# Kernel optimization log

Measured on AMD Instinct MI355X. Metric: run time of the kernel, lower is better.

## Reference

```python
import jax, jax.numpy as jnp
import numpy as np
from jax import lax

N_VOX = 100000   # occupied voxels
GRID = 160       # dense grid extent per axis
K = 5            # kernel size -> 125 offsets
K3 = K * K * K
IMG_C, PTS_C, OUT_C = 64, 32, 16
EPS = 1e-5


def _build_coords_and_kernel_map():
    """Random unique voxel coords + kernel map: nbr[n,k] = row index of voxel at
    coords[n]+offset[k], or N_VOX (sentinel -> zero feature) if unoccupied."""
    rng = np.random.default_rng(0)
    flat = rng.choice(GRID ** 3, size=N_VOX, replace=False)
    coords = np.stack(np.unravel_index(flat, (GRID, GRID, GRID)), axis=1).astype(np.int64)
    B = GRID + 4  # shift coords by +2 so offsets in [-2,2] never wrap
    enc = ((coords[:, 0] + 2) * B + (coords[:, 1] + 2)) * B + (coords[:, 2] + 2)
    order = np.argsort(enc)
    enc_s = enc[order]
    offs = np.stack(np.meshgrid(np.arange(-2, 3), np.arange(-2, 3), np.arange(-2, 3), indexing='ij'), axis=-1).reshape(-1, 3)
    nbr = np.full((N_VOX, K3), N_VOX, dtype=np.int32)
    for k, (dx, dy, dz) in enumerate(offs):
        qe = enc + ((dx * B + dy) * B + dz)
        pos = np.clip(np.searchsorted(enc_s, qe), 0, N_VOX - 1)
        hit = enc_s[pos] == qe
        nbr[:, k] = np.where(hit, order[pos].astype(np.int32), np.int32(N_VOX))
    return nbr


def setup_inputs() -> dict:
    nbr_idx = jnp.asarray(_build_coords_and_kernel_map())
    key = jax.random.key(0)
    ks = jax.random.split(key, 20)
    def w(k, shape, fan):
        return jax.random.normal(k, shape, jnp.float32) * (1.0 / np.sqrt(fan))
    def bn(k0, k1, k2, k3):
        g = jax.random.uniform(k0, (OUT_C,), jnp.float32) + 0.5
        b = jax.random.normal(k1, (OUT_C,), jnp.float32) * 0.1
        m = jax.random.normal(k2, (OUT_C,), jnp.float32) * 0.1
        v = jax.random.uniform(k3, (OUT_C,), jnp.float32) + 0.5
        return g, b, m, v
    bn_img = bn(ks[2], ks[3], ks[4], ks[5])
    bn_pts = bn(ks[7], ks[8], ks[9], ks[10])
    bn_vis = bn(ks[12], ks[13], ks[14], ks[15])
    return {
        'img_voxel_feats': jax.random.normal(ks[0], (N_VOX, IMG_C), jnp.float32),
        'pts_voxel_feats': jax.random.normal(ks[1], (N_VOX, PTS_C), jnp.float32),
        'nbr_idx': nbr_idx,
        'W_img': w(ks[16], (K3, IMG_C, OUT_C), K3 * IMG_C),
        'bn_img_g': bn_img[0], 'bn_img_b': bn_img[1], 'bn_img_m': bn_img[2], 'bn_img_v': bn_img[3],
        'W_pts': w(ks[17], (K3, PTS_C, OUT_C), K3 * PTS_C),
        'bn_pts_g': bn_pts[0], 'bn_pts_b': bn_pts[1], 'bn_pts_m': bn_pts[2], 'bn_pts_v': bn_pts[3],
        'W_vis1': w(ks[18], (K3, 2 * OUT_C, OUT_C), K3 * 2 * OUT_C),
        'bn_vis_g': bn_vis[0], 'bn_vis_b': bn_vis[1], 'bn_vis_m': bn_vis[2], 'bn_vis_v': bn_vis[3],
        'W_vis2': w(ks[19], (OUT_C, 1), OUT_C),
    }


def _sparse_conv(feats, W, nbr_idx):
    # gather-GEMM-scatter sparse conv; sentinel row N -> zero feature
    feats_pad = jnp.concatenate([feats, jnp.zeros((1, feats.shape[1]), feats.dtype)], axis=0)
    init = jnp.zeros((feats.shape[0], W.shape[2]), feats.dtype)
    def step(acc, wk_ik):
        W_k, idx_k = wk_ik  # [Cin,Cout], [N]
        return acc + feats_pad[idx_k] @ W_k, None
    out, _ = lax.scan(step, init, (W, nbr_idx.T))
    return out


def _bn_relu(x, g, b, m, v):
    return jax.nn.relu((x - m) * (g * lax.rsqrt(v + EPS)) + b)


def reference(img_voxel_feats, pts_voxel_feats, nbr_idx,
              W_img, bn_img_g, bn_img_b, bn_img_m, bn_img_v,
              W_pts, bn_pts_g, bn_pts_b, bn_pts_m, bn_pts_v,
              W_vis1, bn_vis_g, bn_vis_b, bn_vis_m, bn_vis_v,
              W_vis2):
    img = _bn_relu(_sparse_conv(img_voxel_feats, W_img, nbr_idx), bn_img_g, bn_img_b, bn_img_m, bn_img_v)
    pts = _bn_relu(_sparse_conv(pts_voxel_feats, W_pts, nbr_idx), bn_pts_g, bn_pts_b, bn_pts_m, bn_pts_v)
    cat = jnp.concatenate([img, pts], axis=1)  # [N, 2*OUT_C]
    h = _bn_relu(_sparse_conv(cat, W_vis1, nbr_idx), bn_vis_g, bn_vis_b, bn_vis_m, bn_vis_v)
    vis_w = jax.nn.sigmoid(h @ W_vis2)  # [N,1]
    return vis_w * img + (1.0 - vis_w) * pts
```

## Files before the change

kernel.cpp:

```cpp
#include <hip/hip_runtime.h>

#define N_VOX 100000
#define K3 125
#define CENTER_K 62
#define CAP 4096
#define EPSF 1e-5f

#define CNT 0
#define PRS 2048
#define ACC (2048 + 2 * 125 * CAP)
#define ACV (ACC + N_VOX * 32)
#define CAT (ACV + N_VOX * 16)

__global__ __launch_bounds__(256) void build_pairs(const int* __restrict__ nbr,
                                                   float* __restrict__ ws)
{
    int* cnt = (int*)(ws + CNT);
    int2* pairs = (int2*)(ws + PRS);
    const int TOT4 = (N_VOX * K3) / 4;
    const int4* n4 = (const int4*)nbr;
    for (int i4 = blockIdx.x * 256 + threadIdx.x; i4 < TOT4; i4 += gridDim.x * 256) {
        int4 v = n4[i4];
        int base = i4 * 4;
        int idxs[4] = {v.x, v.y, v.z, v.w};
        #pragma unroll
        for (int j = 0; j < 4; ++j) {
            int idx = idxs[j];
            int i = base + j;
            int n = i / K3;
            int k = i - n * K3;
            if (idx < N_VOX && k != CENTER_K) {
                int pos = atomicAdd(&cnt[k * 16], 1);
                if (pos < CAP) pairs[(size_t)k * CAP + pos] = make_int2(n, idx);
            }
        }
    }
}

__device__ __forceinline__ void loadFA(float4 (&F)[12], int2 pr,
    const float4* __restrict__ fi4, const float4* __restrict__ fp4, int h)
{
    const float4* fi = fi4 + (size_t)pr.y * 16 + h * 8;
    const float4* fp = fp4 + (size_t)pr.y * 8 + h * 4;
    #pragma unroll
    for (int j = 0; j < 8; ++j) F[j] = fi[j];
    #pragma unroll
    for (int j = 0; j < 4; ++j) F[8 + j] = fp[j];
}

__device__ __forceinline__ void computeFA(const float4 (&F)[12],
    const float (&Wi)[32], const float (&Wp)[16], float& aI, float& aP)
{
    float a0 = 0.f, a1 = 0.f, b0 = 0.f, b1 = 0.f;
    #pragma unroll
    for (int j = 0; j < 4; ++j) {
        float4 f = F[j];
        a0 += f.x*Wi[4*j] + f.y*Wi[4*j+1] + f.z*Wi[4*j+2] + f.w*Wi[4*j+3];
        float4 g = F[4 + j];
        a1 += g.x*Wi[16+4*j] + g.y*Wi[16+4*j+1] + g.z*Wi[16+4*j+2] + g.w*Wi[16+4*j+3];
    }
    #pragma unroll
    for (int j = 0; j < 2; ++j) {
        float4 f = F[8 + j];
        b0 += f.x*Wp[4*j] + f.y*Wp[4*j+1] + f.z*Wp[4*j+2] + f.w*Wp[4*j+3];
        float4 g = F[10 + j];
        b1 += g.x*Wp[8+4*j] + g.y*Wp[8+4*j+1] + g.z*Wp[8+4*j+2] + g.w*Wp[8+4*j+3];
    }
    aI = a0 + a1; aP = b0 + b1;
}

__global__ __launch_bounds__(256) void scatterA(
    const float* __restrict__ fimg, const float* __restrict__ fpts,
    const float* __restrict__ Wimg, const float* __restrict__ Wpts,
    float* __restrict__ ws)
{
    const int k = blockIdx.x;
    const int lane = threadIdx.x & 63;
    const int wv = threadIdx.x >> 6;
    const int s = lane >> 5;
    const int h = (lane >> 4) & 1;
    const int o = lane & 15;

    float Wi[32];
    #pragma unroll
    for (int j = 0; j < 32; ++j) Wi[j] = Wimg[k * 1024 + (h * 32 + j) * 16 + o];
    float Wp[16];
    #pragma unroll
    for (int j = 0; j < 16; ++j) Wp[j] = Wpts[k * 512 + (h * 16 + j) * 16 + o];

    int cnt = ((const int*)(ws + CNT))[k * 16];
    if (cnt > CAP) cnt = CAP;
    const int2* __restrict__ pairs = (const int2*)(ws + PRS) + (size_t)k * CAP;
    float* __restrict__ acc = ws + ACC;
    const float4* __restrict__ fi4 = (const float4*)fimg;
    const float4* __restrict__ fp4 = (const float4*)fpts;

    const int S = gridDim.y * 8;
    int p = (blockIdx.y * 4 + wv) * 2 + s;

    int2 prA = make_int2(0, 0), prB = make_int2(0, 0);
    if (p < cnt) prA = pairs[p];
    if (p + S < cnt) prB = pairs[p + S];
    float4 FA[12], FB[12];
    loadFA(FA, prA, fi4, fp4, h);

    while (p < cnt) {
        {
            int2 prC = make_int2(0, 0);
            if (p + 2 * S < cnt) prC = pairs[p + 2 * S];
            loadFA(FB, prB, fi4, fp4, h);
            float aI, aP;
            computeFA(FA, Wi, Wp, aI, aP);
            aI += __shfl_xor(aI, 16); aP += __shfl_xor(aP, 16);
            atomicAdd(&acc[(size_t)prA.x * 32 + h * 16 + o], h ? aP : aI);
            p += S; prA = prB; prB = prC;
        }
        if (p >= cnt) break;
        {
            int2 prC = make_int2(0, 0);
            if (p + 2 * S < cnt) prC = pairs[p + 2 * S];
            loadFA(FA, prB, fi4, fp4, h);
            float aI, aP;
            computeFA(FB, Wi, Wp, aI, aP);
            aI += __shfl_xor(aI, 16); aP += __shfl_xor(aP, 16);
            atomicAdd(&acc[(size_t)prA.x * 32 + h * 16 + o], h ? aP : aI);
            p += S; prA = prB; prB = prC;
        }
    }
}

__device__ __forceinline__ void loadFV(float4 (&F)[8], int2 pr,
    const float4* __restrict__ c4)
{
    const float4* cr = c4 + (size_t)pr.y * 8;
    #pragma unroll
    for (int j = 0; j < 8; ++j) F[j] = cr[j];
}

__device__ __forceinline__ void computeFV(const float4 (&F)[8],
    const float (&Wv)[32], float& aV)
{
    float a0 = 0.f, a1 = 0.f;
    #pragma unroll
    for (int j = 0; j < 4; ++j) {
        float4 f = F[j];
        a0 += f.x*Wv[4*j] + f.y*Wv[4*j+1] + f.z*Wv[4*j+2] + f.w*Wv[4*j+3];
        float4 g = F[4 + j];
        a1 += g.x*Wv[16+4*j] + g.y*Wv[16+4*j+1] + g.z*Wv[16+4*j+2] + g.w*Wv[16+4*j+3];
    }
    aV = a0 + a1;
}

__global__ __launch_bounds__(256) void scatterV(
    const float* __restrict__ Wvis, float* __restrict__ ws)
{
    const int k = blockIdx.x;
    const int lane = threadIdx.x & 63;
    const int wv = threadIdx.x >> 6;
    const int s = lane >> 4;
    const int o = lane & 15;

    float Wv[32];
    #pragma unroll
    for (int j = 0; j < 32; ++j) Wv[j] = Wvis[k * 512 + j * 16 + o];

    int cnt = ((const int*)(ws + CNT))[k * 16];
    if (cnt > CAP) cnt = CAP;
    const int2* __restrict__ pairs = (const int2*)(ws + PRS) + (size_t)k * CAP;
    const float4* __restrict__ c4 = (const float4*)(ws + CAT);
    float* __restrict__ accV = ws + ACV;

    const int S = gridDim.y * 16;
    int p = (blockIdx.y * 4 + wv) * 4 + s;

    int2 prA = make_int2(0, 0), prB = make_int2(0, 0);
    if (p < cnt) prA = pairs[p];
    if (p + S < cnt) prB = pairs[p + S];
    float4 FA[8], FB[8];
    loadFV(FA, prA, c4);

    while (p < cnt) {
        {
            int2 prC = make_int2(0, 0);
            if (p + 2 * S < cnt) prC = pairs[p + 2 * S];
            loadFV(FB, prB, c4);
            float aV; computeFV(FA, Wv, aV);
            atomicAdd(&accV[(size_t)prA.x * 16 + o], aV);
            p += S; prA = prB; prB = prC;
        }
        if (p >= cnt) break;
        {
            int2 prC = make_int2(0, 0);
            if (p + 2 * S < cnt) prC = pairs[p + 2 * S];
            loadFV(FA, prB, c4);
            float aV; computeFV(FB, Wv, aV);
            atomicAdd(&accV[(size_t)prA.x * 16 + o], aV);
            p += S; prA = prB; prB = prC;
        }
    }
}

__global__ __launch_bounds__(256) void finalizeA(
    const float* __restrict__ fimg, const float* __restrict__ fpts,
    const float* __restrict__ Wimg, const float* __restrict__ Wpts,
    float* __restrict__ ws,
    const float* __restrict__ gi, const float* __restrict__ bi,
    const float* __restrict__ mi, const float* __restrict__ vi,
    const float* __restrict__ gp, const float* __restrict__ bp,
    const float* __restrict__ mp, const float* __restrict__ vp)
{
    int o = threadIdx.x & 15;
    int slot = threadIdx.x >> 4;
    float Wi_r[64];
    #pragma unroll
    for (int c = 0; c < 64; ++c) Wi_r[c] = Wimg[CENTER_K * 1024 + c * 16 + o];
    float Wp_r[32];
    #pragma unroll
    for (int c = 0; c < 32; ++c) Wp_r[c] = Wpts[CENTER_K * 512 + c * 16 + o];
    float sI = gi[o] * rsqrtf(vi[o] + EPSF), bI = bi[o], mI = mi[o];
    float sP = gp[o] * rsqrtf(vp[o] + EPSF), bP = bp[o], mP = mp[o];

    const float4* __restrict__ fi4 = (const float4*)fimg;
    const float4* __restrict__ fp4 = (const float4*)fpts;
    const float* __restrict__ acc = ws + ACC;
    float* __restrict__ cat = ws + CAT;

    for (int n = blockIdx.x * 16 + slot; n < N_VOX; n += gridDim.x * 16) {
        const float4* fr = fi4 + (size_t)n * 16;
        const float4* gr = fp4 + (size_t)n * 8;
        float aI0 = 0.f, aI1 = 0.f, aP0 = 0.f, aP1 = 0.f;
        #pragma unroll
        for (int t = 0; t < 8; ++t) {
            float4 f = fr[t];
            aI0 += f.x*Wi_r[4*t] + f.y*Wi_r[4*t+1] + f.z*Wi_r[4*t+2] + f.w*Wi_r[4*t+3];
            float4 g = fr[8 + t];
            aI1 += g.x*Wi_r[32+4*t] + g.y*Wi_r[32+4*t+1] + g.z*Wi_r[32+4*t+2] + g.w*Wi_r[32+4*t+3];
        }
        #pragma unroll
        for (int t = 0; t < 4; ++t) {
            float4 f = gr[t];
            aP0 += f.x*Wp_r[4*t] + f.y*Wp_r[4*t+1] + f.z*Wp_r[4*t+2] + f.w*Wp_r[4*t+3];
            float4 g = gr[4 + t];
            aP1 += g.x*Wp_r[16+4*t] + g.y*Wp_r[16+4*t+1] + g.z*Wp_r[16+4*t+2] + g.w*Wp_r[16+4*t+3];
        }
        float tI = acc[(size_t)n * 32 + o] + aI0 + aI1;
        float tP = acc[(size_t)n * 32 + 16 + o] + aP0 + aP1;
        cat[(size_t)n * 32 + o]      = fmaxf((tI - mI) * sI + bI, 0.f);
        cat[(size_t)n * 32 + 16 + o] = fmaxf((tP - mP) * sP + bP, 0.f);
    }
}

__global__ __launch_bounds__(256) void finalizeB(
    const float* __restrict__ Wvis, float* __restrict__ ws,
    const float* __restrict__ gv, const float* __restrict__ bv,
    const float* __restrict__ mv, const float* __restrict__ vv,
    const float* __restrict__ w2, float* __restrict__ out)
{
    int o = threadIdx.x & 15;
    int slot = threadIdx.x >> 4;
    float Wv_r[32];
    #pragma unroll
    for (int c = 0; c < 32; ++c) Wv_r[c] = Wvis[CENTER_K * 512 + c * 16 + o];
    float sV = gv[o] * rsqrtf(vv[o] + EPSF), bV = bv[o], mV = mv[o], w2_ = w2[o];

    const float4* __restrict__ c4 = (const float4*)(ws + CAT);
    const float* __restrict__ cat = ws + CAT;
    const float* __restrict__ accV = ws + ACV;

    for (int n = blockIdx.x * 16 + slot; n < N_VOX; n += gridDim.x * 16) {
        const float4* cr = c4 + (size_t)n * 8;
        float a0 = 0.f, a1 = 0.f;
        #pragma unroll
        for (int t = 0; t < 4; ++t) {
            float4 f = cr[t];
            a0 += f.x*Wv_r[4*t] + f.y*Wv_r[4*t+1] + f.z*Wv_r[4*t+2] + f.w*Wv_r[4*t+3];
            float4 g = cr[4 + t];
            a1 += g.x*Wv_r[16+4*t] + g.y*Wv_r[16+4*t+1] + g.z*Wv_r[16+4*t+2] + g.w*Wv_r[16+4*t+3];
        }
        float tV = accV[(size_t)n * 16 + o] + a0 + a1;
        float h = fmaxf((tV - mV) * sV + bV, 0.f);
        float ph = h * w2_;
        ph += __shfl_xor(ph, 1); ph += __shfl_xor(ph, 2);
        ph += __shfl_xor(ph, 4); ph += __shfl_xor(ph, 8);
        float vis = 1.f / (1.f + expf(-ph));
        float xi = cat[(size_t)n * 32 + o];
        float xp = cat[(size_t)n * 32 + 16 + o];
        out[(size_t)n * 16 + o] = vis * xi + (1.f - vis) * xp;
    }
}

extern "C" void kernel_launch(void* const* d_in, const int* in_sizes, int n_in,
                              void* d_out, int out_size, void* d_ws, size_t ws_size,
                              hipStream_t stream) {
    const float* fimg = (const float*)d_in[0];
    const float* fpts = (const float*)d_in[1];
    const int*   nbr  = (const int*)d_in[2];
    const float* Wimg = (const float*)d_in[3];
    const float* gi = (const float*)d_in[4];
    const float* bi = (const float*)d_in[5];
    const float* mi = (const float*)d_in[6];
    const float* vi = (const float*)d_in[7];
    const float* Wpts = (const float*)d_in[8];
    const float* gp = (const float*)d_in[9];
    const float* bp = (const float*)d_in[10];
    const float* mp = (const float*)d_in[11];
    const float* vp = (const float*)d_in[12];
    const float* Wvis = (const float*)d_in[13];
    const float* gv = (const float*)d_in[14];
    const float* bv = (const float*)d_in[15];
    const float* mv = (const float*)d_in[16];
    const float* vv = (const float*)d_in[17];
    const float* w2 = (const float*)d_in[18];
    float* out = (float*)d_out;
    float* ws = (float*)d_ws;

    hipMemsetAsync(ws + CNT, 0, 2048 * sizeof(float), stream);
    hipMemsetAsync(ws + ACC, 0, (size_t)N_VOX * 48 * sizeof(float), stream);

    hipLaunchKernelGGL(build_pairs, dim3(4096), dim3(256), 0, stream, nbr, ws);
    hipLaunchKernelGGL(scatterA, dim3(125, 8), dim3(256), 0, stream,
                       fimg, fpts, Wimg, Wpts, ws);
    hipLaunchKernelGGL(finalizeA, dim3(1024), dim3(256), 0, stream,
                       fimg, fpts, Wimg, Wpts, ws, gi, bi, mi, vi, gp, bp, mp, vp);
    hipLaunchKernelGGL(scatterV, dim3(125, 8), dim3(256), 0, stream, Wvis, ws);
    hipLaunchKernelGGL(finalizeB, dim3(1024), dim3(256), 0, stream,
                       Wvis, ws, gv, bv, mv, vv, w2, out);
}
```

Measured before the change: 205.6 us.

## Split channel reduction across more lanes and quadruple scatter grid for occupancy

In scatterA each pair is now handled by a full wave, with four lane groups each reducing a quarter of the input channels and combining them through two shuffles, instead of half-waves with two groups. scatterV likewise splits its channels across two lane groups. The double-buffered software prefetch of feature rows is dropped, which shrinks register arrays, and launch bounds ask for 8 blocks per SM. The grid y-dimension grows from 8 to 32, so more waves are in flight to hide gather latency. The cost is more shuffles, idle lanes during the atomics, and no explicit prefetch of the next feature row.

```diff
diff --git a/kernel.cpp b/kernel.cpp
--- a/kernel.cpp
+++ b/kernel.cpp
@@ -37,39 +37,7 @@
     }
 }
 
-__device__ __forceinline__ void loadFA(float4 (&F)[12], int2 pr,
-    const float4* __restrict__ fi4, const float4* __restrict__ fp4, int h)
-{
-    const float4* fi = fi4 + (size_t)pr.y * 16 + h * 8;
-    const float4* fp = fp4 + (size_t)pr.y * 8 + h * 4;
-    #pragma unroll
-    for (int j = 0; j < 8; ++j) F[j] = fi[j];
-    #pragma unroll
-    for (int j = 0; j < 4; ++j) F[8 + j] = fp[j];
-}
-
-__device__ __forceinline__ void computeFA(const float4 (&F)[12],
-    const float (&Wi)[32], const float (&Wp)[16], float& aI, float& aP)
-{
-    float a0 = 0.f, a1 = 0.f, b0 = 0.f, b1 = 0.f;
-    #pragma unroll
-    for (int j = 0; j < 4; ++j) {
-        float4 f = F[j];
-        a0 += f.x*Wi[4*j] + f.y*Wi[4*j+1] + f.z*Wi[4*j+2] + f.w*Wi[4*j+3];
-        float4 g = F[4 + j];
-        a1 += g.x*Wi[16+4*j] + g.y*Wi[16+4*j+1] + g.z*Wi[16+4*j+2] + g.w*Wi[16+4*j+3];
-    }
-    #pragma unroll
-    for (int j = 0; j < 2; ++j) {
-        float4 f = F[8 + j];
-        b0 += f.x*Wp[4*j] + f.y*Wp[4*j+1] + f.z*Wp[4*j+2] + f.w*Wp[4*j+3];
-        float4 g = F[10 + j];
-        b1 += g.x*Wp[8+4*j] + g.y*Wp[8+4*j+1] + g.z*Wp[8+4*j+2] + g.w*Wp[8+4*j+3];
-    }
-    aI = a0 + a1; aP = b0 + b1;
-}
-
-__global__ __launch_bounds__(256) void scatterA(
+__global__ __launch_bounds__(256, 8) void scatterA(
     const float* __restrict__ fimg, const float* __restrict__ fpts,
     const float* __restrict__ Wimg, const float* __restrict__ Wpts,
     float* __restrict__ ws)
@@ -77,16 +45,15 @@
     const int k = blockIdx.x;
     const int lane = threadIdx.x & 63;
     const int wv = threadIdx.x >> 6;
-    const int s = lane >> 5;
-    const int h = (lane >> 4) & 1;
+    const int q = lane >> 4;
     const int o = lane & 15;
 
-    float Wi[32];
-    #pragma unroll
-    for (int j = 0; j < 32; ++j) Wi[j] = Wimg[k * 1024 + (h * 32 + j) * 16 + o];
-    float Wp[16];
-    #pragma unroll
-    for (int j = 0; j < 16; ++j) Wp[j] = Wpts[k * 512 + (h * 16 + j) * 16 + o];
+    float Wi[16];
+    #pragma unroll
+    for (int j = 0; j < 16; ++j) Wi[j] = Wimg[k * 1024 + (q * 16 + j) * 16 + o];
+    float Wp[8];
+    #pragma unroll
+    for (int j = 0; j < 8; ++j) Wp[j] = Wpts[k * 512 + (q * 8 + j) * 16 + o];
 
     int cnt = ((const int*)(ws + CNT))[k * 16];
     if (cnt > CAP) cnt = CAP;
@@ -95,74 +62,49 @@
     const float4* __restrict__ fi4 = (const float4*)fimg;
     const float4* __restrict__ fp4 = (const float4*)fpts;
 
-    const int S = gridDim.y * 8;
-    int p = (blockIdx.y * 4 + wv) * 2 + s;
-
-    int2 prA = make_int2(0, 0), prB = make_int2(0, 0);
-    if (p < cnt) prA = pairs[p];
-    if (p + S < cnt) prB = pairs[p + S];
-    float4 FA[12], FB[12];
-    loadFA(FA, prA, fi4, fp4, h);
-
+    const int S = gridDim.y * 4;
+    int p = blockIdx.y * 4 + wv;
+
+    int2 pr = make_int2(0, 0);
+    if (p < cnt) pr = pairs[p];
     while (p < cnt) {
-        {
-            int2 prC = make_int2(0, 0);
-            if (p + 2 * S < cnt) prC = pairs[p + 2 * S];
-            loadFA(FB, prB, fi4, fp4, h);
-            float aI, aP;
-            computeFA(FA, Wi, Wp, aI, aP);
-            aI += __shfl_xor(aI, 16); aP += __shfl_xor(aP, 16);
-            atomicAdd(&acc[(size_t)prA.x * 32 + h * 16 + o], h ? aP : aI);
-            p += S; prA = prB; prB = prC;
-        }
-        if (p >= cnt) break;
-        {
-            int2 prC = make_int2(0, 0);
-            if (p + 2 * S < cnt) prC = pairs[p + 2 * S];
-            loadFA(FA, prB, fi4, fp4, h);
-            float aI, aP;
-            computeFA(FB, Wi, Wp, aI, aP);
-            aI += __shfl_xor(aI, 16); aP += __shfl_xor(aP, 16);
-            atomicAdd(&acc[(size_t)prA.x * 32 + h * 16 + o], h ? aP : aI);
-            p += S; prA = prB; prB = prC;
-        }
-    }
-}
-
-__device__ __forceinline__ void loadFV(float4 (&F)[8], int2 pr,
-    const float4* __restrict__ c4)
-{
-    const float4* cr = c4 + (size_t)pr.y * 8;
-    #pragma unroll
-    for (int j = 0; j < 8; ++j) F[j] = cr[j];
-}
-
-__device__ __forceinline__ void computeFV(const float4 (&F)[8],
-    const float (&Wv)[32], float& aV)
-{
-    float a0 = 0.f, a1 = 0.f;
-    #pragma unroll
-    for (int j = 0; j < 4; ++j) {
-        float4 f = F[j];
-        a0 += f.x*Wv[4*j] + f.y*Wv[4*j+1] + f.z*Wv[4*j+2] + f.w*Wv[4*j+3];
-        float4 g = F[4 + j];
-        a1 += g.x*Wv[16+4*j] + g.y*Wv[16+4*j+1] + g.z*Wv[16+4*j+2] + g.w*Wv[16+4*j+3];
-    }
-    aV = a0 + a1;
-}
-
-__global__ __launch_bounds__(256) void scatterV(
+        int pn = p + S;
+        int2 prn = make_int2(0, 0);
+        if (pn < cnt) prn = pairs[pn];
+        const float4* fr = fi4 + (size_t)pr.y * 16 + q * 4;
+        const float4* gr = fp4 + (size_t)pr.y * 8 + q * 2;
+        float aI = 0.f, aP = 0.f;
+        #pragma unroll
+        for (int j = 0; j < 4; ++j) {
+            float4 f = fr[j];
+            aI += f.x*Wi[4*j] + f.y*Wi[4*j+1] + f.z*Wi[4*j+2] + f.w*Wi[4*j+3];
+        }
+        #pragma unroll
+        for (int j = 0; j < 2; ++j) {
+            float4 f = gr[j];
+            aP += f.x*Wp[4*j] + f.y*Wp[4*j+1] + f.z*Wp[4*j+2] + f.w*Wp[4*j+3];
+        }
+        aI += __shfl_xor(aI, 16); aI += __shfl_xor(aI, 32);
+        aP += __shfl_xor(aP, 16); aP += __shfl_xor(aP, 32);
+        if (lane < 32)
+            atomicAdd(&acc[(size_t)pr.x * 32 + lane], lane < 16 ? aI : aP);
+        p = pn; pr = prn;
+    }
+}
+
+__global__ __launch_bounds__(256, 8) void scatterV(
     const float* __restrict__ Wvis, float* __restrict__ ws)
 {
     const int k = blockIdx.x;
     const int lane = threadIdx.x & 63;
     const int wv = threadIdx.x >> 6;
-    const int s = lane >> 4;
+    const int s = lane >> 5;
+    const int q = (lane >> 4) & 1;
     const int o = lane & 15;
 
-    float Wv[32];
-    #pragma unroll
-    for (int j = 0; j < 32; ++j) Wv[j] = Wvis[k * 512 + j * 16 + o];
+    float Wv[16];
+    #pragma unroll
+    for (int j = 0; j < 16; ++j) Wv[j] = Wvis[k * 512 + (q * 16 + j) * 16 + o];
 
     int cnt = ((const int*)(ws + CNT))[k * 16];
     if (cnt > CAP) cnt = CAP;
@@ -170,33 +112,26 @@
     const float4* __restrict__ c4 = (const float4*)(ws + CAT);
     float* __restrict__ accV = ws + ACV;
 
-    const int S = gridDim.y * 16;
-    int p = (blockIdx.y * 4 + wv) * 4 + s;
-
-    int2 prA = make_int2(0, 0), prB = make_int2(0, 0);
-    if (p < cnt) prA = pairs[p];
-    if (p + S < cnt) prB = pairs[p + S];
-    float4 FA[8], FB[8];
-    loadFV(FA, prA, c4);
-
+    const int S = gridDim.y * 8;
+    int p = (blockIdx.y * 4 + wv) * 2 + s;
+
+    int2 pr = make_int2(0, 0);
+    if (p < cnt) pr = pairs[p];
     while (p < cnt) {
-        {
-            int2 prC = make_int2(0, 0);
-            if (p + 2 * S < cnt) prC = pairs[p + 2 * S];
-            loadFV(FB, prB, c4);
-            float aV; computeFV(FA, Wv, aV);
-            atomicAdd(&accV[(size_t)prA.x * 16 + o], aV);
-            p += S; prA = prB; prB = prC;
-        }
-        if (p >= cnt) break;
-        {
-            int2 prC = make_int2(0, 0);
-            if (p + 2 * S < cnt) prC = pairs[p + 2 * S];
-            loadFV(FA, prB, c4);
-            float aV; computeFV(FB, Wv, aV);
-            atomicAdd(&accV[(size_t)prA.x * 16 + o], aV);
-            p += S; prA = prB; prB = prC;
-        }
+        int pn = p + S;
+        int2 prn = make_int2(0, 0);
+        if (pn < cnt) prn = pairs[pn];
+        const float4* cr = c4 + (size_t)pr.y * 8 + q * 4;
+        float aV = 0.f;
+        #pragma unroll
+        for (int j = 0; j < 4; ++j) {
+            float4 f = cr[j];
+            aV += f.x*Wv[4*j] + f.y*Wv[4*j+1] + f.z*Wv[4*j+2] + f.w*Wv[4*j+3];
+        }
+        aV += __shfl_xor(aV, 16);
+        if (q == 0)
+            atomicAdd(&accV[(size_t)pr.x * 16 + o], aV);
+        p = pn; pr = prn;
     }
 }
 
@@ -318,11 +253,11 @@
     hipMemsetAsync(ws + ACC, 0, (size_t)N_VOX * 48 * sizeof(float), stream);
 
     hipLaunchKernelGGL(build_pairs, dim3(4096), dim3(256), 0, stream, nbr, ws);
-    hipLaunchKernelGGL(scatterA, dim3(125, 8), dim3(256), 0, stream,
+    hipLaunchKernelGGL(scatterA, dim3(125, 32), dim3(256), 0, stream,
                        fimg, fpts, Wimg, Wpts, ws);
     hipLaunchKernelGGL(finalizeA, dim3(1024), dim3(256), 0, stream,
                        fimg, fpts, Wimg, Wpts, ws, gi, bi, mi, vi, gp, bp, mp, vp);
-    hipLaunchKernelGGL(scatterV, dim3(125, 8), dim3(256), 0, stream, Wvis, ws);
+    hipLaunchKernelGGL(scatterV, dim3(125, 32), dim3(256), 0, stream, Wvis, ws);
     hipLaunchKernelGGL(finalizeB, dim3(1024), dim3(256), 0, stream,
                        Wvis, ws, gv, bv, mv, vv, w2, out);
 }
```

After: 214.2 us. 1.04x slower.
